# Kernel optimization log

Hardware: AMD Instinct MI355X
Metric: run time of the kernel (lower is better)

Reference implementation:

```python
import jax, jax.numpy as jnp
import numpy as np

TAU = 2.0          # LIF membrane time constant (spikingjelly default)
V_TH = 1.0         # v_threshold
V_RESET = 0.0      # hard reset value
ATAN_ALPHA = 2.0   # surrogate.ATan default alpha
EPS = 1e-12        # F.normalize eps

@jax.custom_vjp
def spike_fn(x):
    # Heaviside forward, ATan surrogate backward
    return (x >= 0).astype(x.dtype)

def _spike_fwd(x):
    return spike_fn(x), x

def _spike_bwd(x, g):
    sg = (ATAN_ALPHA / 2.0) / (1.0 + (jnp.pi / 2.0 * ATAN_ALPHA * x) ** 2)
    return (g * sg,)

spike_fn.defvjp(_spike_fwd, _spike_bwd)

def setup_inputs() -> dict:
    key = jax.random.key(0)
    k1, k2 = jax.random.split(key)
    T, B, F, H = 32, 512, 2048, 2048
    x_seq = jax.random.normal(k1, (T, B, F), dtype=jnp.float32)
    lim = float(np.sqrt(6.0 / (F + H)))  # xavier_uniform
    W = jax.random.uniform(k2, (H, F), dtype=jnp.float32, minval=-lim, maxval=lim)
    b = jnp.zeros((H,), dtype=jnp.float32)
    return {"x_seq": x_seq, "W": W, "b": b}

def reference(x_seq, W, b):
    # Linear: [T,B,F] @ [F,H] -> [T,B,H]
    cur = jnp.einsum('tbf,hf->tbh', x_seq, W) + b
    # F.normalize(dim=-1): L2 normalize the injected current per neuron vector
    norm = jnp.maximum(jnp.sqrt(jnp.sum(cur * cur, axis=-1, keepdims=True)), EPS)
    cur = cur / norm

    def step(v, c):
        # LIF charge: v <- v + (x - (v - v_reset)) / tau
        v = v + (c - (v - V_RESET)) / TAU
        s = spike_fn(v - V_TH)
        sd = jax.lax.stop_gradient(s)  # detach_reset=True
        v = v * (1.0 - sd) + V_RESET * sd  # hard reset
        return v, s

    v0 = jnp.zeros(cur.shape[1:], dtype=cur.dtype)  # [B,H]
    _, spk_seq = jax.lax.scan(step, v0, cur)  # spk_seq: [T,B,H]
    count = spk_seq.sum(axis=0)  # [B,H]
    return spk_seq, count
```

## Files before the change

### kernel.cpp

```cpp
#include <hip/hip_runtime.h>
#include <hip/hip_bf16.h>

#define T_SZ 32
#define B_SZ 512
#define F_SZ 2048
#define H_SZ 2048
#define M_SZ (T_SZ * B_SZ)

typedef short bf16x8 __attribute__((ext_vector_type(8)));
typedef float f32x4  __attribute__((ext_vector_type(4)));
typedef unsigned short u16x8 __attribute__((ext_vector_type(8)));

__device__ __forceinline__ void gload_lds16(const void* g, void* l) {
    __builtin_amdgcn_global_load_lds(
        (const __attribute__((address_space(1))) unsigned int*)g,
        (__attribute__((address_space(3))) unsigned int*)l,
        16, 0, 0);
}

__global__ __launch_bounds__(256) void cvt_bf16_kernel(const float* __restrict__ in,
                                                       unsigned short* __restrict__ out,
                                                       int n4) {
    int i = blockIdx.x * 256 + threadIdx.x;
    if (i >= n4) return;
    float4 v = ((const float4*)in)[i];
    ushort4 o;
    o.x = __builtin_bit_cast(unsigned short, __float2bfloat16(v.x));
    o.y = __builtin_bit_cast(unsigned short, __float2bfloat16(v.y));
    o.z = __builtin_bit_cast(unsigned short, __float2bfloat16(v.z));
    o.w = __builtin_bit_cast(unsigned short, __float2bfloat16(v.w));
    ((ushort4*)out)[i] = o;
}

__global__ __launch_bounds__(256) void gemm_bt_kernel(const __hip_bfloat16* __restrict__ A,
                                                      const __hip_bfloat16* __restrict__ Bt,
                                                      const float* __restrict__ bias,
                                                      __hip_bfloat16* __restrict__ C)
{
    __shared__ __align__(16) __hip_bfloat16 As[128 * 32];
    __shared__ __align__(16) __hip_bfloat16 Bs[128 * 32];

    const int tid  = threadIdx.x;
    const int lane = tid & 63;
    const int wave = tid >> 6;
    const int wm   = wave >> 1;
    const int wn   = wave & 1;
    const int m0   = blockIdx.y * 128;
    const int n0   = blockIdx.x * 128;
    const int quad = lane >> 4;
    const int r16  = lane & 15;

    f32x4 acc[4][4] = {};

    for (int k0 = 0; k0 < F_SZ; k0 += 32) {
        __syncthreads();
        #pragma unroll
        for (int j = 0; j < 2; ++j) {
            int chunk = j * 256 + tid;
            int row   = chunk >> 2;
            int kp    = (chunk & 3) << 3;
            gload_lds16(A  + (size_t)(m0 + row) * F_SZ + k0 + kp, (void*)(As + chunk * 8));
            gload_lds16(Bt + (size_t)(n0 + row) * F_SZ + k0 + kp, (void*)(Bs + chunk * 8));
        }
        __syncthreads();

        bf16x8 af[4], bq[4];
        #pragma unroll
        for (int i = 0; i < 4; ++i) {
            af[i] = *(const bf16x8*)(As + (wm * 64 + i * 16 + r16) * 32 + quad * 8);
            bq[i] = *(const bf16x8*)(Bs + (wn * 64 + i * 16 + r16) * 32 + quad * 8);
        }
        #pragma unroll
        for (int mi = 0; mi < 4; ++mi)
            #pragma unroll
            for (int ni = 0; ni < 4; ++ni)
                acc[mi][ni] = __builtin_amdgcn_mfma_f32_16x16x32_bf16(af[mi], bq[ni], acc[mi][ni], 0, 0, 0);
    }

    #pragma unroll
    for (int ni = 0; ni < 4; ++ni) {
        const int gn = n0 + wn * 64 + ni * 16 + r16;
        const float bv = bias[gn];
        #pragma unroll
        for (int mi = 0; mi < 4; ++mi) {
            const int gm = m0 + wm * 64 + mi * 16 + quad * 4;
            #pragma unroll
            for (int r = 0; r < 4; ++r)
                C[(size_t)(gm + r) * H_SZ + gn] = __float2bfloat16(acc[mi][ni][r] + bv);
        }
    }
}

__global__ __launch_bounds__(256) void norm_lif_kernel(const __hip_bfloat16* __restrict__ cur,
                                                       float* __restrict__ spk,
                                                       float* __restrict__ cnt)
{
    const int b    = blockIdx.x;
    const int tid  = threadIdx.x;
    const int lane = tid & 63;
    const int wv   = tid >> 6;

    __shared__ float wred[T_SZ][4];
    __shared__ float ninv[T_SZ];

    float ss[T_SZ];
    #pragma unroll
    for (int t = 0; t < T_SZ; ++t) {
        const u16x8 pk = *(const u16x8*)(cur + (size_t)(t * B_SZ + b) * H_SZ + tid * 8);
        float s = 0.f;
        #pragma unroll
        for (int j = 0; j < 8; ++j) {
            float f = __uint_as_float(((unsigned)pk[j]) << 16);
            s += f * f;
        }
        ss[t] = s;
    }
    #pragma unroll
    for (int t = 0; t < T_SZ; ++t) {
        float s = ss[t];
        #pragma unroll
        for (int off = 32; off >= 1; off >>= 1) s += __shfl_down(s, off, 64);
        if (lane == 0) wred[t][wv] = s;
    }
    __syncthreads();
    if (tid < T_SZ) {
        float s = wred[tid][0] + wred[tid][1] + wred[tid][2] + wred[tid][3];
        ninv[tid] = 1.0f / fmaxf(sqrtf(s), 1e-12f);
    }
    __syncthreads();

    float v[8]   = {0, 0, 0, 0, 0, 0, 0, 0};
    float cn8[8] = {0, 0, 0, 0, 0, 0, 0, 0};
    #pragma unroll
    for (int t = 0; t < T_SZ; ++t) {
        const size_t off = (size_t)(t * B_SZ + b) * H_SZ + tid * 8;
        const u16x8 pk = *(const u16x8*)(cur + off);
        const float inv = ninv[t];
        float so[8];
        #pragma unroll
        for (int j = 0; j < 8; ++j) {
            float c = __uint_as_float(((unsigned)pk[j]) << 16) * inv;
            v[j] += (c - v[j]) * 0.5f;
            float s = (v[j] >= 1.0f) ? 1.0f : 0.0f;
            so[j] = s;
            cn8[j] += s;
            v[j] = (s != 0.f) ? 0.f : v[j];
        }
        *(float4*)(spk + off)     = make_float4(so[0], so[1], so[2], so[3]);
        *(float4*)(spk + off + 4) = make_float4(so[4], so[5], so[6], so[7]);
    }
    const size_t coff = (size_t)b * H_SZ + tid * 8;
    *(float4*)(cnt + coff)     = make_float4(cn8[0], cn8[1], cn8[2], cn8[3]);
    *(float4*)(cnt + coff + 4) = make_float4(cn8[4], cn8[5], cn8[6], cn8[7]);
}

extern "C" void kernel_launch(void* const* d_in, const int* in_sizes, int n_in,
                              void* d_out, int out_size, void* d_ws, size_t ws_size,
                              hipStream_t stream) {
    const float* x    = (const float*)d_in[0];
    const float* W    = (const float*)d_in[1];
    const float* bias = (const float*)d_in[2];

    float* spk = (float*)d_out;
    float* cnt = spk + (size_t)T_SZ * B_SZ * H_SZ;

    char* ws = (char*)d_ws;
    __hip_bfloat16* xb   = (__hip_bfloat16*)ws;
    __hip_bfloat16* Wb   = (__hip_bfloat16*)(ws + (size_t)M_SZ * F_SZ * 2);
    __hip_bfloat16* curb = (__hip_bfloat16*)(ws + (size_t)M_SZ * F_SZ * 2
                                                + (size_t)H_SZ * F_SZ * 2);

    cvt_bf16_kernel<<<(M_SZ * F_SZ) / 1024, 256, 0, stream>>>(x, (unsigned short*)xb, (M_SZ * F_SZ) / 4);
    cvt_bf16_kernel<<<(H_SZ * F_SZ) / 1024, 256, 0, stream>>>(W, (unsigned short*)Wb, (H_SZ * F_SZ) / 4);
    gemm_bt_kernel<<<dim3(H_SZ / 128, M_SZ / 128), 256, 0, stream>>>(xb, Wb, bias, curb);
    norm_lif_kernel<<<B_SZ, 256, 0, stream>>>(curb, spk, cnt);
}
```

Measured before the change: 427.7 us.

## Split norm+LIF into row-sum-of-squares kernel and wider-grid LIF scan kernel

Replaces the single norm_lif kernel, which ran only 512 blocks, with two kernels. The first computes a per-row inverse L2 norm using one wave per row across 4096 blocks. The second runs the LIF scan with 4 neurons per thread across 1024 blocks. The goal is better occupancy and parallelism on the memory-bound tail, at the cost of an extra launch and re-reading cur from global memory.

```diff
diff --git a/kernel.cpp b/kernel.cpp
--- a/kernel.cpp
+++ b/kernel.cpp
@@ -16,6 +16,10 @@
         (const __attribute__((address_space(1))) unsigned int*)g,
         (__attribute__((address_space(3))) unsigned int*)l,
         16, 0, 0);
+}
+
+__device__ __forceinline__ float bf16_bits_to_f32(unsigned short u) {
+    return __uint_as_float(((unsigned)u) << 16);
 }
 
 __global__ __launch_bounds__(256) void cvt_bf16_kernel(const float* __restrict__ in,
@@ -91,67 +95,61 @@
     }
 }
 
-__global__ __launch_bounds__(256) void norm_lif_kernel(const __hip_bfloat16* __restrict__ cur,
+__global__ __launch_bounds__(256) void row_ss_kernel(const __hip_bfloat16* __restrict__ cur,
+                                                     float* __restrict__ ninv) {
+    const int lane = threadIdx.x & 63;
+    const int row  = blockIdx.x * 4 + (threadIdx.x >> 6);
+    const __hip_bfloat16* rp = cur + (size_t)row * H_SZ;
+
+    float s = 0.f;
+    #pragma unroll
+    for (int i = 0; i < 4; ++i) {
+        const u16x8 pk = *(const u16x8*)(rp + i * 512 + lane * 8);
+        #pragma unroll
+        for (int j = 0; j < 8; ++j) {
+            float f = bf16_bits_to_f32(pk[j]);
+            s += f * f;
+        }
+    }
+    #pragma unroll
+    for (int off = 32; off >= 1; off >>= 1) s += __shfl_down(s, off, 64);
+    if (lane == 0) ninv[row] = 1.0f / fmaxf(sqrtf(s), 1e-12f);
+}
+
+__global__ __launch_bounds__(256) void lif_scan_kernel(const __hip_bfloat16* __restrict__ cur,
+                                                       const float* __restrict__ ninv,
                                                        float* __restrict__ spk,
                                                        float* __restrict__ cnt)
 {
-    const int b    = blockIdx.x;
-    const int tid  = threadIdx.x;
-    const int lane = tid & 63;
-    const int wv   = tid >> 6;
+    const int gid = blockIdx.x * 256 + threadIdx.x;
+    const int b   = gid >> 9;
+    const int h0  = (gid & 511) * 4;
 
-    __shared__ float wred[T_SZ][4];
-    __shared__ float ninv[T_SZ];
-
-    float ss[T_SZ];
+    float v[4]  = {0, 0, 0, 0};
+    float cn[4] = {0, 0, 0, 0};
     #pragma unroll
     for (int t = 0; t < T_SZ; ++t) {
-        const u16x8 pk = *(const u16x8*)(cur + (size_t)(t * B_SZ + b) * H_SZ + tid * 8);
-        float s = 0.f;
+        const size_t off = (size_t)(t * B_SZ + b) * H_SZ + h0;
+        const ushort4 pk = *(const ushort4*)(cur + off);
+        const float inv  = ninv[t * B_SZ + b];
+        float so[4];
+        {
+            float c;
+            c = bf16_bits_to_f32(pk.x) * inv; v[0] += (c - v[0]) * 0.5f;
+            c = bf16_bits_to_f32(pk.y) * inv; v[1] += (c - v[1]) * 0.5f;
+            c = bf16_bits_to_f32(pk.z) * inv; v[2] += (c - v[2]) * 0.5f;
+            c = bf16_bits_to_f32(pk.w) * inv; v[3] += (c - v[3]) * 0.5f;
+        }
         #pragma unroll
-        for (int j = 0; j < 8; ++j) {
-            float f = __uint_as_float(((unsigned)pk[j]) << 16);
-            s += f * f;
-        }
-        ss[t] = s;
-    }
-    #pragma unroll
-    for (int t = 0; t < T_SZ; ++t) {
-        float s = ss[t];
-        #pragma unroll
-        for (int off = 32; off >= 1; off >>= 1) s += __shfl_down(s, off, 64);
-        if (lane == 0) wred[t][wv] = s;
-    }
-    __syncthreads();
-    if (tid < T_SZ) {
-        float s = wred[tid][0] + wred[tid][1] + wred[tid][2] + wred[tid][3];
-        ninv[tid] = 1.0f / fmaxf(sqrtf(s), 1e-12f);
-    }
-    __syncthreads();
-
-    float v[8]   = {0, 0, 0, 0, 0, 0, 0, 0};
-    float cn8[8] = {0, 0, 0, 0, 0, 0, 0, 0};
-    #pragma unroll
-    for (int t = 0; t < T_SZ; ++t) {
-        const size_t off = (size_t)(t * B_SZ + b) * H_SZ + tid * 8;
-        const u16x8 pk = *(const u16x8*)(cur + off);
-        const float inv = ninv[t];
-        float so[8];
-        #pragma unroll
-        for (int j = 0; j < 8; ++j) {
-            float c = __uint_as_float(((unsigned)pk[j]) << 16) * inv;
-            v[j] += (c - v[j]) * 0.5f;
+        for (int j = 0; j < 4; ++j) {
             float s = (v[j] >= 1.0f) ? 1.0f : 0.0f;
             so[j] = s;
-            cn8[j] += s;
+            cn[j] += s;
             v[j] = (s != 0.f) ? 0.f : v[j];
         }
-        *(float4*)(spk + off)     = make_float4(so[0], so[1], so[2], so[3]);
-        *(float4*)(spk + off + 4) = make_float4(so[4], so[5], so[6], so[7]);
+        *(float4*)(spk + off) = make_float4(so[0], so[1], so[2], so[3]);
     }
-    const size_t coff = (size_t)b * H_SZ + tid * 8;
-    *(float4*)(cnt + coff)     = make_float4(cn8[0], cn8[1], cn8[2], cn8[3]);
-    *(float4*)(cnt + coff + 4) = make_float4(cn8[4], cn8[5], cn8[6], cn8[7]);
+    *(float4*)(cnt + (size_t)b * H_SZ + h0) = make_float4(cn[0], cn[1], cn[2], cn[3]);
 }
 
 extern "C" void kernel_launch(void* const* d_in, const int* in_sizes, int n_in,
@@ -169,9 +167,13 @@
     __hip_bfloat16* Wb   = (__hip_bfloat16*)(ws + (size_t)M_SZ * F_SZ * 2);
     __hip_bfloat16* curb = (__hip_bfloat16*)(ws + (size_t)M_SZ * F_SZ * 2
                                                 + (size_t)H_SZ * F_SZ * 2);
+    float* ninv          = (float*)(ws + (size_t)M_SZ * F_SZ * 2
+                                       + (size_t)H_SZ * F_SZ * 2
+                                       + (size_t)M_SZ * H_SZ * 2);
 
     cvt_bf16_kernel<<<(M_SZ * F_SZ) / 1024, 256, 0, stream>>>(x, (unsigned short*)xb, (M_SZ * F_SZ) / 4);
     cvt_bf16_kernel<<<(H_SZ * F_SZ) / 1024, 256, 0, stream>>>(W, (unsigned short*)Wb, (H_SZ * F_SZ) / 4);
     gemm_bt_kernel<<<dim3(H_SZ / 128, M_SZ / 128), 256, 0, stream>>>(xb, Wb, bias, curb);
-    norm_lif_kernel<<<B_SZ, 256, 0, stream>>>(curb, spk, cnt);
+    row_ss_kernel<<<M_SZ / 4, 256, 0, stream>>>(curb, ninv);
+    lif_scan_kernel<<<(B_SZ * H_SZ / 4) / 256, 256, 0, stream>>>(curb, ninv, spk, cnt);
 }
```

After: 430.5 us. About the same (+0.7%).
